# Optimization experiments

Hardware: AMD Instinct MI355X
Metric: run time of the kernel (lower is better)

## Reference

```python
import jax, jax.numpy as jnp
import numpy as np

B, S, H, D = 2, 2048, 2048, 256  # batch, seq, hidden, head_dim
NH, NKV = 8, 1                   # attention heads, kv heads
N_REP = NH // NKV
SCALING = D ** -0.5
ROPE_THETA = 10000.0
NEG_INF = -1e9


def rotate_half(x):
    x1, x2 = jnp.split(x, 2, axis=-1)
    return jnp.concatenate((-x2, x1), axis=-1)


def setup_inputs() -> dict:
    key = jax.random.key(0)
    ks = jax.random.split(key, 5)
    hidden_states = jax.random.normal(ks[0], (B, S, H), dtype=jnp.float32)
    # RoPE cos/sin per position, Gemma-style: inv_freq tiled over full head_dim
    inv_freq = 1.0 / (ROPE_THETA ** (np.arange(0, D, 2, dtype=np.float32) / D))  # [D/2]
    pos = np.arange(S, dtype=np.float32)
    freqs = np.outer(pos, inv_freq)                      # [S, D/2]
    emb = np.concatenate([freqs, freqs], axis=-1)        # [S, D]
    cos = jnp.broadcast_to(jnp.asarray(np.cos(emb)), (B, S, D))
    sin = jnp.broadcast_to(jnp.asarray(np.sin(emb)), (B, S, D))
    # additive causal mask [B, 1, S, S]
    causal = jnp.triu(jnp.full((S, S), NEG_INF, dtype=jnp.float32), k=1)
    attention_mask = jnp.broadcast_to(causal[None, None], (B, 1, S, S))
    scale = 0.02
    Wq = jax.random.normal(ks[1], (H, NH * D), dtype=jnp.float32) * scale
    Wk = jax.random.normal(ks[2], (H, NKV * D), dtype=jnp.float32) * scale
    Wv = jax.random.normal(ks[3], (H, NKV * D), dtype=jnp.float32) * scale
    Wo = jax.random.normal(ks[4], (NH * D, H), dtype=jnp.float32) * scale
    return {"hidden_states": hidden_states, "cos": cos, "sin": sin,
            "attention_mask": attention_mask, "Wq": Wq, "Wk": Wk, "Wv": Wv, "Wo": Wo}


def reference(hidden_states, cos, sin, attention_mask, Wq, Wk, Wv, Wo):
    # projections: [B,S,H] @ [H, nh*D] -> [B, nh, S, D]
    q = (hidden_states @ Wq).reshape(B, S, NH, D).transpose(0, 2, 1, 3)
    k = (hidden_states @ Wk).reshape(B, S, NKV, D).transpose(0, 2, 1, 3)
    v = (hidden_states @ Wv).reshape(B, S, NKV, D).transpose(0, 2, 1, 3)
    # RoPE (cos/sin broadcast over head dim via unsqueeze at axis 1)
    c = cos[:, None]  # [B,1,S,D]
    s = sin[:, None]
    q = q * c + rotate_half(q) * s
    k = k * c + rotate_half(k) * s
    # repeat_kv: [B, NKV, S, D] -> [B, NH, S, D]
    k = jnp.repeat(k, N_REP, axis=1)
    v = jnp.repeat(v, N_REP, axis=1)
    # eager attention
    attn_weights = jnp.einsum("bhqd,bhkd->bhqk", q, k) * SCALING
    attn_weights = attn_weights + attention_mask[:, :, :, :S]
    attn_weights = jax.nn.softmax(attn_weights.astype(jnp.float32), axis=-1).astype(q.dtype)
    attn_output = jnp.einsum("bhqk,bhkd->bhqd", attn_weights, v)
    attn_output = attn_output.transpose(0, 2, 1, 3).reshape(B, S, NH * D)
    attn_output = attn_output @ Wo
    return attn_output, attn_weights
```

## Files before the change

### kernel.cpp

```cpp
#include <hip/hip_runtime.h>
#include <hip/hip_bf16.h>

#define B_   2
#define S_   2048
#define H_   2048
#define D_   256
#define NH_  8

typedef unsigned short u16;
typedef __bf16 bf16x8 __attribute__((ext_vector_type(8)));
typedef float f32x4 __attribute__((ext_vector_type(4)));
typedef unsigned int uint4v __attribute__((ext_vector_type(4)));
typedef unsigned int uint2v __attribute__((ext_vector_type(2)));

#define AS1 __attribute__((address_space(1)))
#define AS3 __attribute__((address_space(3)))

__device__ __forceinline__ u16 f2bf(float x) {
  union { float f; unsigned u; } v; v.f = x;
  unsigned u = v.u;
  u += 0x7FFFu + ((u >> 16) & 1u);
  return (u16)(u >> 16);
}
__device__ __forceinline__ float bf2f(u16 x) {
  union { unsigned u; float f; } v; v.u = ((unsigned)x) << 16;
  return v.f;
}

__device__ __forceinline__ void gld_lds16(const u16* g, u16* l) {
  __builtin_amdgcn_global_load_lds((const AS1 unsigned int*)g,
                                   (AS3 unsigned int*)l, 16, 0, 0);
}

#define BM 128
#define BN 128
#define BK 32

enum GemmMode { MODE_PROJ = 0, MODE_QK = 1, MODE_PV = 2, MODE_WO = 3 };

template <int MODE>
__global__ __launch_bounds__(256)
void gemm_nt(const u16* __restrict__ A, const u16* __restrict__ Bb,
             void* __restrict__ Cp, float* __restrict__ rows,
             int K, int lda, int ldb, int ldc)
{
  const int bn = blockIdx.x, bm = blockIdx.y, bz = blockIdx.z;
  if (MODE == MODE_QK && bn > bm) return;
  const int m0 = bm * BM, n0 = bn * BN;

  const u16* Ap = A;
  const u16* Bp = Bb;
  float* Cf = (float*)Cp;
  u16*   Cu = (u16*)Cp;

  if constexpr (MODE == MODE_QK) {
    Ap   += (size_t)bz * S_ * D_;
    Bp   += (size_t)(bz >> 3) * S_ * D_;
    Cu   += (size_t)bz * S_ * S_;
    rows += (size_t)bz * S_;
  } else if constexpr (MODE == MODE_PV) {
    Ap   += (size_t)bz * S_ * S_;
    Bp   += (size_t)(bz >> 3) * D_ * S_;
    Cu   += (size_t)(bz >> 3) * S_ * (NH_ * D_) + (size_t)(bz & 7) * D_;
    rows += (size_t)bz * S_;
  }

  int Keff = K;
  if constexpr (MODE == MODE_PV) {
    int lim = (bm + 1) * BM;
    Keff = lim < K ? lim : K;
  }

  __shared__ __align__(16) u16 As[BM * BK];
  __shared__ __align__(16) u16 Bs[BN * BK];

  const int tid  = threadIdx.x;
  const int lane = tid & 63;
  const int quad = lane >> 4;
  const int l16  = lane & 15;
  const int wave = tid >> 6;
  const int wm   = (wave >> 1) << 6;
  const int wn   = (wave & 1) << 6;

  f32x4 acc[4][4] = {};

  for (int kt = 0; kt < Keff; kt += BK) {
    #pragma unroll
    for (int i = 0; i < 2; i++) {
      int c = tid + i * 256;
      gld_lds16(Ap + (size_t)(m0 + (c >> 2)) * lda + kt + (c & 3) * 8, &As[c * 8]);
    }
    #pragma unroll
    for (int i = 0; i < 2; i++) {
      int c = tid + i * 256;
      gld_lds16(Bp + (size_t)(n0 + (c >> 2)) * ldb + kt + (c & 3) * 8, &Bs[c * 8]);
    }
    __syncthreads();

    bf16x8 af[4], bfr[4];
    #pragma unroll
    for (int i = 0; i < 4; i++)
      af[i] = *(const bf16x8*)(&As[(wm + i * 16 + l16) * BK + quad * 8]);
    #pragma unroll
    for (int j = 0; j < 4; j++)
      bfr[j] = *(const bf16x8*)(&Bs[(wn + j * 16 + l16) * BK + quad * 8]);
    #pragma unroll
    for (int i = 0; i < 4; i++)
      #pragma unroll
      for (int j = 0; j < 4; j++)
        acc[i][j] = __builtin_amdgcn_mfma_f32_16x16x32_bf16(af[i], bfr[j], acc[i][j], 0, 0, 0);
    __syncthreads();
  }

  const float SCL2 = 0.0625f * 1.44269504088896340736f;
  #pragma unroll
  for (int i = 0; i < 4; i++) {
    #pragma unroll
    for (int r = 0; r < 4; r++) {
      const int m = m0 + wm + i * 16 + quad * 4 + r;
      if constexpr (MODE == MODE_QK) {
        float rs = 0.f;
        #pragma unroll
        for (int j = 0; j < 4; j++) {
          int n = n0 + wn + j * 16 + l16;
          float e = (n <= m) ? exp2f(acc[i][j][r] * SCL2) : 0.f;
          rs += e;
          Cu[(size_t)m * ldc + n] = f2bf(e);
        }
        #pragma unroll
        for (int o = 1; o < 16; o <<= 1) rs += __shfl_xor(rs, o, 64);
        if (l16 == 0) atomicAdd(&rows[m], rs);
      } else if constexpr (MODE == MODE_PV) {
        float inv = 1.0f / rows[m];
        #pragma unroll
        for (int j = 0; j < 4; j++) {
          int n = n0 + wn + j * 16 + l16;
          Cu[(size_t)m * ldc + n] = f2bf(acc[i][j][r] * inv);
        }
      } else if constexpr (MODE == MODE_WO) {
        #pragma unroll
        for (int j = 0; j < 4; j++) {
          int n = n0 + wn + j * 16 + l16;
          Cf[(size_t)m * ldc + n] = acc[i][j][r];
        }
      } else {
        #pragma unroll
        for (int j = 0; j < 4; j++) {
          int n = n0 + wn + j * 16 + l16;
          Cu[(size_t)m * ldc + n] = f2bf(acc[i][j][r]);
        }
      }
    }
  }
}

__global__ __launch_bounds__(256)
void convert_bf16_kernel(const float* __restrict__ src, u16* __restrict__ dst, int n4)
{
  int i = blockIdx.x * 256 + threadIdx.x;
  if (i >= n4) return;
  float4 f = ((const float4*)src)[i];
  uint2v p;
  p.x = (unsigned)f2bf(f.x) | ((unsigned)f2bf(f.y) << 16);
  p.y = (unsigned)f2bf(f.z) | ((unsigned)f2bf(f.w) << 16);
  ((uint2v*)dst)[i] = p;
}

__global__ __launch_bounds__(256)
void transpose_convert(const float* __restrict__ src, u16* __restrict__ dst, int K, int N)
{
  __shared__ float t[32][33];
  int n0 = blockIdx.x * 32, k0 = blockIdx.y * 32;
  int c = threadIdx.x & 31, r = threadIdx.x >> 5;
  #pragma unroll
  for (int rr = 0; rr < 32; rr += 8)
    t[r + rr][c] = src[(size_t)(k0 + r + rr) * N + n0 + c];
  __syncthreads();
  #pragma unroll
  for (int rr = 0; rr < 32; rr += 8)
    dst[(size_t)(n0 + r + rr) * K + k0 + c] = f2bf(t[c][r + rr]);
}

__global__ __launch_bounds__(256)
void transpose_v_kernel(const u16* __restrict__ v, u16* __restrict__ vt)
{
  __shared__ u16 t[32][34];
  int b = blockIdx.z;
  int d0 = blockIdx.x * 32, s0 = blockIdx.y * 32;
  int c = threadIdx.x & 31, r = threadIdx.x >> 5;
  #pragma unroll
  for (int rr = 0; rr < 32; rr += 8)
    t[r + rr][c] = v[(size_t)(b * S_ + s0 + r + rr) * 2560 + 2304 + d0 + c];
  __syncthreads();
  #pragma unroll
  for (int rr = 0; rr < 32; rr += 8)
    vt[(size_t)b * D_ * S_ + (size_t)(d0 + r + rr) * S_ + s0 + c] = t[c][r + rr];
}

__global__ __launch_bounds__(256)
void rope_q_kernel(const u16* __restrict__ qraw, const float* __restrict__ cosb,
                   const float* __restrict__ sinb, u16* __restrict__ qout)
{
  int idx = blockIdx.x;
  int h = idx & 7, bs = idx >> 3;
  int b = bs >> 11, s = bs & (S_ - 1);
  int d = threadIdx.x;
  size_t base = (size_t)bs * 2560 + (size_t)h * D_;
  float qv = bf2f(qraw[base + d]);
  float qp = bf2f(qraw[base + (d ^ 128)]);
  float c  = cosb[(size_t)bs * D_ + d];
  float sn = sinb[(size_t)bs * D_ + d];
  float rot = (d < 128) ? -qp : qp;
  qout[(((size_t)b * NH_ + h) * S_ + s) * D_ + d] = f2bf(qv * c + rot * sn);
}

__global__ __launch_bounds__(256)
void rope_k_kernel(const u16* __restrict__ kraw, const float* __restrict__ cosb,
                   const float* __restrict__ sinb, u16* __restrict__ kout)
{
  int bs = blockIdx.x;
  int d = threadIdx.x;
  size_t base = (size_t)bs * 2560 + 2048;
  float kv = bf2f(kraw[base + d]);
  float kp = bf2f(kraw[base + (d ^ 128)]);
  float c  = cosb[(size_t)bs * D_ + d];
  float sn = sinb[(size_t)bs * D_ + d];
  float rot = (d < 128) ? -kp : kp;
  kout[(size_t)bs * D_ + d] = f2bf(kv * c + rot * sn);
}

__global__ __launch_bounds__(256)
void normalize_p(const u16* __restrict__ E, const float* __restrict__ rows,
                 float* __restrict__ P)
{
  const int r = blockIdx.x;
  const int q = r & (S_ - 1);
  const u16* e = E + (size_t)r * S_;
  float* p = P + (size_t)r * S_;
  const float inv = 1.0f / rows[r];
  const int k0 = threadIdx.x * 8;

  float4 lo = {0.f, 0.f, 0.f, 0.f}, hi = {0.f, 0.f, 0.f, 0.f};
  if (k0 <= q) {
    uint4v u = *(const uint4v*)(e + k0);
    float v[8];
    v[0] = bf2f(u.x & 0xffff); v[1] = bf2f(u.x >> 16);
    v[2] = bf2f(u.y & 0xffff); v[3] = bf2f(u.y >> 16);
    v[4] = bf2f(u.z & 0xffff); v[5] = bf2f(u.z >> 16);
    v[6] = bf2f(u.w & 0xffff); v[7] = bf2f(u.w >> 16);
    lo.x = (k0 + 0 <= q) ? v[0] * inv : 0.f;
    lo.y = (k0 + 1 <= q) ? v[1] * inv : 0.f;
    lo.z = (k0 + 2 <= q) ? v[2] * inv : 0.f;
    lo.w = (k0 + 3 <= q) ? v[3] * inv : 0.f;
    hi.x = (k0 + 4 <= q) ? v[4] * inv : 0.f;
    hi.y = (k0 + 5 <= q) ? v[5] * inv : 0.f;
    hi.z = (k0 + 6 <= q) ? v[6] * inv : 0.f;
    hi.w = (k0 + 7 <= q) ? v[7] * inv : 0.f;
  }
  *(float4*)(p + k0)     = lo;
  *(float4*)(p + k0 + 4) = hi;
}

extern "C" void kernel_launch(void* const* d_in, const int* in_sizes, int n_in,
                              void* d_out, int out_size, void* d_ws, size_t ws_size,
                              hipStream_t stream)
{
  const float* X    = (const float*)d_in[0];
  const float* cosb = (const float*)d_in[1];
  const float* sinb = (const float*)d_in[2];
  const float* Wq   = (const float*)d_in[4];
  const float* Wk   = (const float*)d_in[5];
  const float* Wv   = (const float*)d_in[6];
  const float* Wo   = (const float*)d_in[7];

  float* outO = (float*)d_out;
  float* outP = outO + (size_t)B_ * S_ * H_;

  u16* ws     = (u16*)d_ws;
  u16* Xbf    = ws;
  u16* WT     = Xbf    + 8388608;
  u16* WoT    = WT     + 5242880;
  u16* QKVraw = WoT    + 4194304;
  u16* Qbf    = QKVraw + 10485760;
  u16* Kbf    = Qbf    + 8388608;
  u16* VT     = Kbf    + 1048576;
  u16* AObf   = VT     + 1048576;
  u16* Ebf    = AObf   + 8388608;
  float* Rows = (float*)(Ebf + 67108864);

  convert_bf16_kernel<<<8192, 256, 0, stream>>>(X, Xbf, 2097152);
  transpose_convert<<<dim3(64, 64), 256, 0, stream>>>(Wq, WT, 2048, 2048);
  transpose_convert<<<dim3(8, 64),  256, 0, stream>>>(Wk, WT + 2048 * 2048, 2048, 256);
  transpose_convert<<<dim3(8, 64),  256, 0, stream>>>(Wv, WT + 2304 * 2048, 2048, 256);
  transpose_convert<<<dim3(64, 64), 256, 0, stream>>>(Wo, WoT, 2048, 2048);
  gemm_nt<MODE_PROJ><<<dim3(20, 32, 1), 256, 0, stream>>>(
      Xbf, WT, QKVraw, nullptr, 2048, 2048, 2048, 2560);
  rope_q_kernel<<<32768, 256, 0, stream>>>(QKVraw, cosb, sinb, Qbf);
  rope_k_kernel<<<4096, 256, 0, stream>>>(QKVraw, cosb, sinb, Kbf);
  transpose_v_kernel<<<dim3(8, 64, 2), 256, 0, stream>>>(QKVraw, VT);
  hipMemsetAsync(Rows, 0, 32768 * sizeof(float), stream);
  gemm_nt<MODE_QK><<<dim3(16, 16, 16), 256, 0, stream>>>(
      Qbf, Kbf, Ebf, Rows, 256, 256, 256, 2048);
  normalize_p<<<32768, 256, 0, stream>>>(Ebf, Rows, outP);
  gemm_nt<MODE_PV><<<dim3(2, 16, 16), 256, 0, stream>>>(
      Ebf, VT, AObf, Rows, 2048, 2048, 2048, 2048);
  gemm_nt<MODE_WO><<<dim3(16, 32, 1), 256, 0, stream>>>(
      AObf, WoT, outO, nullptr, 2048, 2048, 2048, 2048);
}
```

Before: 709.3 us.

## Compact causal QK grid, stage bf16 epilogue via LDS, batch elementwise kernels

After: 694.2 us. -2.1%, faster.

```diff
diff --git a/kernel.cpp b/kernel.cpp
--- a/kernel.cpp
+++ b/kernel.cpp
@@ -44,8 +44,20 @@
              void* __restrict__ Cp, float* __restrict__ rows,
              int K, int lda, int ldb, int ldc)
 {
-  const int bn = blockIdx.x, bm = blockIdx.y, bz = blockIdx.z;
-  if (MODE == MODE_QK && bn > bm) return;
+  int bn, bm;
+  if constexpr (MODE == MODE_QK) {
+    int t = blockIdx.x;
+    bm = 0;
+    while ((bm + 1) * (bm + 2) / 2 <= t) bm++;
+    bn = t - bm * (bm + 1) / 2;
+  } else if constexpr (MODE == MODE_PV) {
+    bn = blockIdx.x;
+    bm = (int)gridDim.y - 1 - (int)blockIdx.y;
+  } else {
+    bn = blockIdx.x;
+    bm = blockIdx.y;
+  }
+  const int bz = blockIdx.z;
   const int m0 = bm * BM, n0 = bn * BN;
 
   const u16* Ap = A;
@@ -113,43 +125,60 @@
   }
 
   const float SCL2 = 0.0625f * 1.44269504088896340736f;
-  #pragma unroll
-  for (int i = 0; i < 4; i++) {
-    #pragma unroll
-    for (int r = 0; r < 4; r++) {
-      const int m = m0 + wm + i * 16 + quad * 4 + r;
-      if constexpr (MODE == MODE_QK) {
-        float rs = 0.f;
-        #pragma unroll
-        for (int j = 0; j < 4; j++) {
-          int n = n0 + wn + j * 16 + l16;
-          float e = (n <= m) ? exp2f(acc[i][j][r] * SCL2) : 0.f;
-          rs += e;
-          Cu[(size_t)m * ldc + n] = f2bf(e);
-        }
-        #pragma unroll
-        for (int o = 1; o < 16; o <<= 1) rs += __shfl_xor(rs, o, 64);
-        if (l16 == 0) atomicAdd(&rows[m], rs);
-      } else if constexpr (MODE == MODE_PV) {
-        float inv = 1.0f / rows[m];
-        #pragma unroll
-        for (int j = 0; j < 4; j++) {
-          int n = n0 + wn + j * 16 + l16;
-          Cu[(size_t)m * ldc + n] = f2bf(acc[i][j][r] * inv);
-        }
-      } else if constexpr (MODE == MODE_WO) {
+  if constexpr (MODE == MODE_WO) {
+    #pragma unroll
+    for (int i = 0; i < 4; i++) {
+      #pragma unroll
+      for (int r = 0; r < 4; r++) {
+        const int m = m0 + wm + i * 16 + quad * 4 + r;
         #pragma unroll
         for (int j = 0; j < 4; j++) {
           int n = n0 + wn + j * 16 + l16;
           Cf[(size_t)m * ldc + n] = acc[i][j][r];
         }
-      } else {
-        #pragma unroll
-        for (int j = 0; j < 4; j++) {
-          int n = n0 + wn + j * 16 + l16;
-          Cu[(size_t)m * ldc + n] = f2bf(acc[i][j][r]);
+      }
+    }
+  } else {
+    __shared__ __align__(16) u16 Cs[32][136];
+    const int band16 = (wave >> 1) * 16;
+    #pragma unroll
+    for (int i = 0; i < 4; i++) {
+      #pragma unroll
+      for (int r = 0; r < 4; r++) {
+        const int lr = band16 + quad * 4 + r;
+        const int m  = m0 + wm + i * 16 + quad * 4 + r;
+        if constexpr (MODE == MODE_QK) {
+          float rs = 0.f;
+          #pragma unroll
+          for (int j = 0; j < 4; j++) {
+            int n = n0 + wn + j * 16 + l16;
+            float e = (n <= m) ? exp2f(acc[i][j][r] * SCL2) : 0.f;
+            rs += e;
+            Cs[lr][wn + j * 16 + l16] = f2bf(e);
+          }
+          #pragma unroll
+          for (int o = 1; o < 16; o <<= 1) rs += __shfl_xor(rs, o, 64);
+          if (l16 == 0) atomicAdd(&rows[m], rs);
+        } else if constexpr (MODE == MODE_PV) {
+          const float inv = 1.0f / rows[m];
+          #pragma unroll
+          for (int j = 0; j < 4; j++)
+            Cs[lr][wn + j * 16 + l16] = f2bf(acc[i][j][r] * inv);
+        } else {
+          #pragma unroll
+          for (int j = 0; j < 4; j++)
+            Cs[lr][wn + j * 16 + l16] = f2bf(acc[i][j][r]);
         }
       }
+      __syncthreads();
+      #pragma unroll
+      for (int ch = tid; ch < 512; ch += 256) {
+        const int rr = ch >> 4, cc = ch & 15;
+        const int mg = m0 + ((rr >> 4) << 6) + i * 16 + (rr & 15);
+        *(uint4v*)(Cu + (size_t)mg * ldc + n0 + cc * 8) =
+            *(const uint4v*)(&Cs[rr][cc * 8]);
+      }
+      __syncthreads();
     }
   }
 }
@@ -157,13 +186,16 @@
 __global__ __launch_bounds__(256)
 void convert_bf16_kernel(const float* __restrict__ src, u16* __restrict__ dst, int n4)
 {
-  int i = blockIdx.x * 256 + threadIdx.x;
-  if (i >= n4) return;
-  float4 f = ((const float4*)src)[i];
-  uint2v p;
-  p.x = (unsigned)f2bf(f.x) | ((unsigned)f2bf(f.y) << 16);
-  p.y = (unsigned)f2bf(f.z) | ((unsigned)f2bf(f.w) << 16);
-  ((uint2v*)dst)[i] = p;
+  #pragma unroll
+  for (int it = 0; it < 4; ++it) {
+    int i = it * 524288 + blockIdx.x * 256 + threadIdx.x;
+    if (i >= n4) return;
+    float4 f = ((const float4*)src)[i];
+    uint2v p;
+    p.x = (unsigned)f2bf(f.x) | ((unsigned)f2bf(f.y) << 16);
+    p.y = (unsigned)f2bf(f.z) | ((unsigned)f2bf(f.w) << 16);
+    ((uint2v*)dst)[i] = p;
+  }
 }
 
 __global__ __launch_bounds__(256)
@@ -201,64 +233,75 @@
 void rope_q_kernel(const u16* __restrict__ qraw, const float* __restrict__ cosb,
                    const float* __restrict__ sinb, u16* __restrict__ qout)
 {
-  int idx = blockIdx.x;
-  int h = idx & 7, bs = idx >> 3;
-  int b = bs >> 11, s = bs & (S_ - 1);
-  int d = threadIdx.x;
-  size_t base = (size_t)bs * 2560 + (size_t)h * D_;
-  float qv = bf2f(qraw[base + d]);
-  float qp = bf2f(qraw[base + (d ^ 128)]);
-  float c  = cosb[(size_t)bs * D_ + d];
-  float sn = sinb[(size_t)bs * D_ + d];
-  float rot = (d < 128) ? -qp : qp;
-  qout[(((size_t)b * NH_ + h) * S_ + s) * D_ + d] = f2bf(qv * c + rot * sn);
+  const int d    = threadIdx.x & 127;
+  const int half = threadIdx.x >> 7;
+  #pragma unroll
+  for (int it = 0; it < 16; ++it) {
+    int idx = blockIdx.x * 32 + it * 2 + half;
+    int h = idx & 7, bs = idx >> 3;
+    int b = bs >> 11, s = bs & (S_ - 1);
+    size_t base = (size_t)bs * 2560 + (size_t)h * D_;
+    float q1 = bf2f(qraw[base + d]);
+    float q2 = bf2f(qraw[base + 128 + d]);
+    float c  = cosb[(size_t)bs * D_ + d];
+    float sn = sinb[(size_t)bs * D_ + d];
+    size_t ob = (((size_t)b * NH_ + h) * S_ + s) * D_;
+    qout[ob + d]       = f2bf(q1 * c - q2 * sn);
+    qout[ob + 128 + d] = f2bf(q2 * c + q1 * sn);
+  }
 }
 
 __global__ __launch_bounds__(256)
 void rope_k_kernel(const u16* __restrict__ kraw, const float* __restrict__ cosb,
                    const float* __restrict__ sinb, u16* __restrict__ kout)
 {
-  int bs = blockIdx.x;
-  int d = threadIdx.x;
-  size_t base = (size_t)bs * 2560 + 2048;
-  float kv = bf2f(kraw[base + d]);
-  float kp = bf2f(kraw[base + (d ^ 128)]);
-  float c  = cosb[(size_t)bs * D_ + d];
-  float sn = sinb[(size_t)bs * D_ + d];
-  float rot = (d < 128) ? -kp : kp;
-  kout[(size_t)bs * D_ + d] = f2bf(kv * c + rot * sn);
+  const int d    = threadIdx.x & 127;
+  const int half = threadIdx.x >> 7;
+  #pragma unroll
+  for (int it = 0; it < 8; ++it) {
+    int bs = blockIdx.x * 16 + it * 2 + half;
+    size_t base = (size_t)bs * 2560 + 2048;
+    float k1 = bf2f(kraw[base + d]);
+    float k2 = bf2f(kraw[base + 128 + d]);
+    float c  = cosb[(size_t)bs * D_ + d];
+    float sn = sinb[(size_t)bs * D_ + d];
+    kout[(size_t)bs * D_ + d]       = f2bf(k1 * c - k2 * sn);
+    kout[(size_t)bs * D_ + 128 + d] = f2bf(k2 * c + k1 * sn);
+  }
 }
 
 __global__ __launch_bounds__(256)
 void normalize_p(const u16* __restrict__ E, const float* __restrict__ rows,
                  float* __restrict__ P)
 {
-  const int r = blockIdx.x;
-  const int q = r & (S_ - 1);
-  const u16* e = E + (size_t)r * S_;
-  float* p = P + (size_t)r * S_;
-  const float inv = 1.0f / rows[r];
   const int k0 = threadIdx.x * 8;
-
-  float4 lo = {0.f, 0.f, 0.f, 0.f}, hi = {0.f, 0.f, 0.f, 0.f};
-  if (k0 <= q) {
-    uint4v u = *(const uint4v*)(e + k0);
-    float v[8];
-    v[0] = bf2f(u.x & 0xffff); v[1] = bf2f(u.x >> 16);
-    v[2] = bf2f(u.y & 0xffff); v[3] = bf2f(u.y >> 16);
-    v[4] = bf2f(u.z & 0xffff); v[5] = bf2f(u.z >> 16);
-    v[6] = bf2f(u.w & 0xffff); v[7] = bf2f(u.w >> 16);
-    lo.x = (k0 + 0 <= q) ? v[0] * inv : 0.f;
-    lo.y = (k0 + 1 <= q) ? v[1] * inv : 0.f;
-    lo.z = (k0 + 2 <= q) ? v[2] * inv : 0.f;
-    lo.w = (k0 + 3 <= q) ? v[3] * inv : 0.f;
-    hi.x = (k0 + 4 <= q) ? v[4] * inv : 0.f;
-    hi.y = (k0 + 5 <= q) ? v[5] * inv : 0.f;
-    hi.z = (k0 + 6 <= q) ? v[6] * inv : 0.f;
-    hi.w = (k0 + 7 <= q) ? v[7] * inv : 0.f;
-  }
-  *(float4*)(p + k0)     = lo;
-  *(float4*)(p + k0 + 4) = hi;
+  for (int rr = 0; rr < 16; ++rr) {
+    const int r = blockIdx.x * 16 + rr;
+    const int q = r & (S_ - 1);
+    const u16* e = E + (size_t)r * S_;
+    float* p = P + (size_t)r * S_;
+    const float inv = 1.0f / rows[r];
+
+    float4 lo = {0.f, 0.f, 0.f, 0.f}, hi = {0.f, 0.f, 0.f, 0.f};
+    if (k0 <= q) {
+      uint4v u = *(const uint4v*)(e + k0);
+      float v[8];
+      v[0] = bf2f(u.x & 0xffff); v[1] = bf2f(u.x >> 16);
+      v[2] = bf2f(u.y & 0xffff); v[3] = bf2f(u.y >> 16);
+      v[4] = bf2f(u.z & 0xffff); v[5] = bf2f(u.z >> 16);
+      v[6] = bf2f(u.w & 0xffff); v[7] = bf2f(u.w >> 16);
+      lo.x = (k0 + 0 <= q) ? v[0] * inv : 0.f;
+      lo.y = (k0 + 1 <= q) ? v[1] * inv : 0.f;
+      lo.z = (k0 + 2 <= q) ? v[2] * inv : 0.f;
+      lo.w = (k0 + 3 <= q) ? v[3] * inv : 0.f;
+      hi.x = (k0 + 4 <= q) ? v[4] * inv : 0.f;
+      hi.y = (k0 + 5 <= q) ? v[5] * inv : 0.f;
+      hi.z = (k0 + 6 <= q) ? v[6] * inv : 0.f;
+      hi.w = (k0 + 7 <= q) ? v[7] * inv : 0.f;
+    }
+    *(float4*)(p + k0)     = lo;
+    *(float4*)(p + k0 + 4) = hi;
+  }
 }
 
 extern "C" void kernel_launch(void* const* d_in, const int* in_sizes, int n_in,
@@ -288,20 +331,20 @@
   u16* Ebf    = AObf   + 8388608;
   float* Rows = (float*)(Ebf + 67108864);
 
-  convert_bf16_kernel<<<8192, 256, 0, stream>>>(X, Xbf, 2097152);
+  convert_bf16_kernel<<<2048, 256, 0, stream>>>(X, Xbf, 2097152);
   transpose_convert<<<dim3(64, 64), 256, 0, stream>>>(Wq, WT, 2048, 2048);
   transpose_convert<<<dim3(8, 64),  256, 0, stream>>>(Wk, WT + 2048 * 2048, 2048, 256);
   transpose_convert<<<dim3(8, 64),  256, 0, stream>>>(Wv, WT + 2304 * 2048, 2048, 256);
   transpose_convert<<<dim3(64, 64), 256, 0, stream>>>(Wo, WoT, 2048, 2048);
   gemm_nt<MODE_PROJ><<<dim3(20, 32, 1), 256, 0, stream>>>(
       Xbf, WT, QKVraw, nullptr, 2048, 2048, 2048, 2560);
-  rope_q_kernel<<<32768, 256, 0, stream>>>(QKVraw, cosb, sinb, Qbf);
-  rope_k_kernel<<<4096, 256, 0, stream>>>(QKVraw, cosb, sinb, Kbf);
+  rope_q_kernel<<<1024, 256, 0, stream>>>(QKVraw, cosb, sinb, Qbf);
+  rope_k_kernel<<<256, 256, 0, stream>>>(QKVraw, cosb, sinb, Kbf);
   transpose_v_kernel<<<dim3(8, 64, 2), 256, 0, stream>>>(QKVraw, VT);
   hipMemsetAsync(Rows, 0, 32768 * sizeof(float), stream);
-  gemm_nt<MODE_QK><<<dim3(16, 16, 16), 256, 0, stream>>>(
+  gemm_nt<MODE_QK><<<dim3(136, 1, 16), 256, 0, stream>>>(
       Qbf, Kbf, Ebf, Rows, 256, 256, 256, 2048);
-  normalize_p<<<32768, 256, 0, stream>>>(Ebf, Rows, outP);
+  normalize_p<<<2048, 256, 0, stream>>>(Ebf, Rows, outP);
   gemm_nt<MODE_PV><<<dim3(2, 16, 16), 256, 0, stream>>>(
       Ebf, VT, AObf, Rows, 2048, 2048, 2048, 2048);
   gemm_nt<MODE_WO><<<dim3(16, 32, 1), 256, 0, stream>>>(
```
